# Kernel tuning notes

Hardware: AMD Instinct MI355X
Metric: run time of the kernel (lower is better)

## Reference

```python
import jax, jax.numpy as jnp
import numpy as np

N_NODES = 100000
N_EDGES = 1600000
HIDDEN = 128


def setup_inputs() -> dict:
    key = jax.random.key(0)
    ks = jax.random.split(key, 10)
    inp = {
        "hidden_states": jax.random.normal(ks[0], (N_NODES, HIDDEN), dtype=jnp.float32),
        "edges_i": jax.random.randint(ks[1], (2, N_EDGES), 0, N_NODES, dtype=jnp.int64),
        "edges_ii": jax.random.randint(ks[2], (2, N_EDGES), 0, N_NODES, dtype=jnp.int64),
        "edges_iii": jax.random.randint(ks[3], (2, N_EDGES), 0, N_NODES, dtype=jnp.int64),
        "edges_a": jax.random.randint(ks[4], (2, N_EDGES), 0, N_NODES, dtype=jnp.int64),
        # GCNConv weights (hidden -> hidden), no bias, Glorot-like init
        "W_i": jax.random.normal(ks[5], (HIDDEN, HIDDEN), dtype=jnp.float32) / np.sqrt(HIDDEN),
        "W_ii": jax.random.normal(ks[6], (HIDDEN, HIDDEN), dtype=jnp.float32) / np.sqrt(HIDDEN),
        "W_iii": jax.random.normal(ks[7], (HIDDEN, HIDDEN), dtype=jnp.float32) / np.sqrt(HIDDEN),
        "W_a": jax.random.normal(ks[8], (HIDDEN, HIDDEN), dtype=jnp.float32) / np.sqrt(HIDDEN),
    }
    return inp


def _gcn_conv(x, W, edges):
    # GCNConv with normalize=False, add_self_loops=False, bias=False:
    # out[dst] = sum over edges (x @ W)[src]
    xw = x @ W                                   # [N, H] small GEMM
    msg = jnp.take(xw, edges[0], axis=0)         # gather at src: [E, H]
    return jax.ops.segment_sum(msg, edges[1], num_segments=x.shape[0])


def reference(hidden_states, edges_i, edges_ii, edges_iii, edges_a, W_i, W_ii, W_iii, W_a):
    # VariationalNormalEpanechnikovDropout acts as identity in eval mode.
    x = hidden_states
    out = _gcn_conv(x, W_i, edges_i)
    out = out + _gcn_conv(x, W_ii, edges_ii)
    out = out + _gcn_conv(x, W_iii, edges_iii)
    out = out + _gcn_conv(x, W_a, edges_a)
    return out
```

## Files before the change

### kernel.cpp

```cpp
#include <hip/hip_runtime.h>


#define H 128
#define BSH 9
#define BNODES (1 << BSH)
#define SEGB (BNODES * 4)
#define EPB 16384

typedef __bf16 bf16x8 __attribute__((ext_vector_type(8)));
typedef float f32x4 __attribute__((ext_vector_type(4)));

static __device__ __forceinline__ ushort f2bf(float f) {
  union { float f; uint u; } v; v.f = f;
  uint r = (v.u + 0x7FFFu + ((v.u >> 16) & 1u)) >> 16;
  return (ushort)r;
}
static __device__ __forceinline__ float bflo(uint u) {
  union { uint u; float f; } v; v.u = u << 16; return v.f;
}
static __device__ __forceinline__ float bfhi(uint u) {
  union { uint u; float f; } v; v.u = u & 0xFFFF0000u; return v.f;
}

__global__ __launch_bounds__(256) void conv_prep(const float4* __restrict__ X4,
                                                 uint2* __restrict__ Xb2, int m,
                                                 const float* __restrict__ W0,
                                                 const float* __restrict__ W1,
                                                 const float* __restrict__ W2,
                                                 const float* __restrict__ W3,
                                                 ushort* __restrict__ Wt) {
  int i = blockIdx.x * 256 + threadIdx.x;
  if (i < m) {
    float4 v = X4[i];
    uint2 p;
    p.x = (uint)f2bf(v.x) | ((uint)f2bf(v.y) << 16);
    p.y = (uint)f2bf(v.z) | ((uint)f2bf(v.w) << 16);
    Xb2[i] = p;
  }
  if (i < 65536) {
    int kk = i & 127;
    int c = (i >> 7) & 127;
    int k = i >> 14;
    const float* W = (k == 0) ? W0 : (k == 1) ? W1 : (k == 2) ? W2 : W3;
    Wt[i] = f2bf(W[kk * 128 + c]);
  }
}

static __device__ __forceinline__ void fetch_edge(
    int gid, int c1, int c2, int c3,
    const int* d0, const int* d1, const int* d2, const int* d3,
    const int* s0, const int* s1, const int* s2, const int* s3,
    int& dst, int& src, int& k) {
  int i;
  const int *dp, *sp;
  if (gid < c1)      { k = 0; i = gid;      dp = d0; sp = s0; }
  else if (gid < c2) { k = 1; i = gid - c1; dp = d1; sp = s1; }
  else if (gid < c3) { k = 2; i = gid - c2; dp = d2; sp = s2; }
  else               { k = 3; i = gid - c3; dp = d3; sp = s3; }
  dst = dp[i];
  src = sp[i];
}

__global__ __launch_bounds__(256) void part_count(
    const int* __restrict__ d0, const int* __restrict__ d1,
    const int* __restrict__ d2, const int* __restrict__ d3,
    int c1, int c2, int c3, int tot, int nbin, int* __restrict__ hb) {
  __shared__ int lh[512];
  for (int i = threadIdx.x; i < nbin; i += 256) lh[i] = 0;
  __syncthreads();
  int base = blockIdx.x * EPB;
#pragma unroll 8
  for (int u = 0; u < EPB / 256; ++u) {
    int gid = base + u * 256 + threadIdx.x;
    if (gid < tot) {
      int i;
      const int* dp;
      if (gid < c1)      { i = gid;      dp = d0; }
      else if (gid < c2) { i = gid - c1; dp = d1; }
      else if (gid < c3) { i = gid - c2; dp = d2; }
      else               { i = gid - c3; dp = d3; }
      atomicAdd(&lh[dp[i] >> BSH], 1);
    }
  }
  __syncthreads();
  int* row = hb + (size_t)blockIdx.x * nbin;
  for (int i = threadIdx.x; i < nbin; i += 256) row[i] = lh[i];
}

__global__ __launch_bounds__(256) void part_scanA(int* __restrict__ hb,
                                                  int nblk, int nbin,
                                                  int* __restrict__ btot) {
  __shared__ int ws4[4];
  const int bin = blockIdx.x;
  const int t = threadIdx.x, lane = t & 63, wid = t >> 6;
  const int C = (nblk + 255) / 256;
  int b0 = t * C;
  int b1 = min(b0 + C, nblk);
  int s = 0;
  for (int b = b0; b < b1; ++b) s += hb[(size_t)b * nbin + bin];
  int incl = s;
#pragma unroll
  for (int d = 1; d < 64; d <<= 1) {
    int x = __shfl_up(incl, d, 64);
    if (lane >= d) incl += x;
  }
  if (lane == 63) ws4[wid] = incl;
  __syncthreads();
  if (t == 0) {
    int run = 0;
#pragma unroll
    for (int i = 0; i < 4; ++i) { int v = ws4[i]; ws4[i] = run; run += v; }
  }
  __syncthreads();
  int run = ws4[wid] + (incl - s);
  for (int b = b0; b < b1; ++b) {
    int v = hb[(size_t)b * nbin + bin];
    hb[(size_t)b * nbin + bin] = run;
    run += v;
  }
  if (t == 255) btot[bin] = run;
}

__global__ __launch_bounds__(512) void part_scanB(const int* __restrict__ btot,
                                                  int* __restrict__ binbase,
                                                  int nbin) {
  __shared__ int ws8[8];
  const int t = threadIdx.x, lane = t & 63, wid = t >> 6;
  int v = (t < nbin) ? btot[t] : 0;
  int incl = v;
#pragma unroll
  for (int d = 1; d < 64; d <<= 1) {
    int x = __shfl_up(incl, d, 64);
    if (lane >= d) incl += x;
  }
  if (lane == 63) ws8[wid] = incl;
  __syncthreads();
  if (t == 0) {
    int run = 0;
#pragma unroll
    for (int i = 0; i < 8; ++i) { int v2 = ws8[i]; ws8[i] = run; run += v2; }
  }
  __syncthreads();
  int excl = ws8[wid] + (incl - v);
  if (t < nbin) binbase[t] = excl;
  if (t == nbin - 1) binbase[nbin] = excl + v;
}

__global__ __launch_bounds__(256) void part_scatter(
    const int* __restrict__ d0, const int* __restrict__ d1,
    const int* __restrict__ d2, const int* __restrict__ d3,
    const int* __restrict__ s0, const int* __restrict__ s1,
    const int* __restrict__ s2, const int* __restrict__ s3,
    int c1, int c2, int c3, int tot, int nbin,
    const int* __restrict__ hb, const int* __restrict__ binbase,
    uint* __restrict__ part) {
  __shared__ int cur[512];
  const int* row = hb + (size_t)blockIdx.x * nbin;
  for (int i = threadIdx.x; i < nbin; i += 256) cur[i] = binbase[i] + row[i];
  __syncthreads();
  int base = blockIdx.x * EPB;
#pragma unroll 8
  for (int u = 0; u < EPB / 256; ++u) {
    int gid = base + u * 256 + threadIdx.x;
    if (gid < tot) {
      int dst, src, k;
      fetch_edge(gid, c1, c2, c3, d0, d1, d2, d3, s0, s1, s2, s3, dst, src, k);
      int pos = atomicAdd(&cur[dst >> BSH], 1);
      part[pos] = (uint)src | ((uint)(((dst & (BNODES - 1)) << 2) | k) << 17);
    }
  }
}

__global__ __launch_bounds__(1024) void build_bucket(
    const uint* __restrict__ part, const int* __restrict__ binbase,
    int* __restrict__ rp4, int* __restrict__ col_idx) {
  __shared__ int lh[SEGB];
  __shared__ int ws16[16];
  const int b = blockIdx.x;
  const int beg = binbase[b], end = binbase[b + 1];
  const int t = threadIdx.x, lane = t & 63, wid = t >> 6;

  lh[t] = 0;
  lh[t + 1024] = 0;
  __syncthreads();
  for (int i = beg + t; i < end; i += 1024)
    atomicAdd(&lh[part[i] >> 17], 1);
  __syncthreads();

  int v0 = lh[2 * t], v1 = lh[2 * t + 1];
  int s = v0 + v1;
  int incl = s;
#pragma unroll
  for (int d = 1; d < 64; d <<= 1) {
    int x = __shfl_up(incl, d, 64);
    if (lane >= d) incl += x;
  }
  if (lane == 63) ws16[wid] = incl;
  __syncthreads();
  if (t == 0) {
    int run = 0;
#pragma unroll
    for (int i = 0; i < 16; ++i) { int w = ws16[i]; ws16[i] = run; run += w; }
  }
  __syncthreads();
  int excl = beg + ws16[wid] + (incl - s);
  lh[2 * t] = excl;
  lh[2 * t + 1] = excl + v0;

  int gseg = b * SEGB + 2 * t;
  rp4[gseg] = excl;
  rp4[gseg + 1] = excl + v0;
  __syncthreads();

  for (int i = beg + t; i < end; i += 1024) {
    uint e = part[i];
    int pos = atomicAdd(&lh[e >> 17], 1);
    col_idx[pos] = (int)(e & 0x1FFFFu);
  }
}

#define ACC8(u)                                                       \
  do {                                                                \
    a0 += bflo((u).x); a1 += bfhi((u).x);                             \
    a2 += bflo((u).y); a3 += bfhi((u).y);                             \
    a4 += bflo((u).z); a5 += bfhi((u).z);                             \
    a6 += bflo((u).w); a7 += bfhi((u).w);                             \
  } while (0)

__global__ __launch_bounds__(256, 8) void gg(const uint* __restrict__ Xb,
                                             const int* __restrict__ rp4,
                                             const int* __restrict__ col_idx,
                                             const ushort* __restrict__ Wt,
                                             float* __restrict__ out, int n) {
  __shared__ uint sS[16][258];

  const int node0 = blockIdx.x * 16;
  const int wave = threadIdx.x >> 6;
  const int lane = threadIdx.x & 63;
  const int g = lane >> 4;
  const int qb = (lane & 15) * 4;

#pragma unroll 1
  for (int i = 0; i < 4; ++i) {
    int local = wave * 4 + i;
    int node = node0 + local;
    if (node < n) {
      const int4 rpv = *(const int4*)(rp4 + (size_t)node * 4);
      const int rpE = rp4[(size_t)node * 4 + 4];
      int pe0 = (rpv.x + lane < rpv.y) ? col_idx[rpv.x + lane] : 0;
      int pe1 = (rpv.y + lane < rpv.z) ? col_idx[rpv.y + lane] : 0;
      int pe2 = (rpv.z + lane < rpv.w) ? col_idx[rpv.z + lane] : 0;
      int pe3 = (rpv.w + lane < rpE)   ? col_idx[rpv.w + lane] : 0;
#pragma unroll
      for (int k = 0; k < 4; ++k) {
        int beg = (k == 0) ? rpv.x : (k == 1) ? rpv.y : (k == 2) ? rpv.z : rpv.w;
        int end = (k == 0) ? rpv.y : (k == 1) ? rpv.z : (k == 2) ? rpv.w : rpE;
        int pe  = (k == 0) ? pe0   : (k == 1) ? pe1   : (k == 2) ? pe2   : pe3;
        int len = end - beg;
        int m = (len > 64) ? 64 : len;
        float a0 = 0.f, a1 = 0.f, a2 = 0.f, a3 = 0.f;
        float a4 = 0.f, a5 = 0.f, a6 = 0.f, a7 = 0.f;
        int s = 0;
        for (; s + 16 <= m; s += 16) {
          int ea = __shfl(pe, s + g, 64);
          int eb = __shfl(pe, s + 4 + g, 64);
          int ec = __shfl(pe, s + 8 + g, 64);
          int ed = __shfl(pe, s + 12 + g, 64);
          uint4 ua = *(const uint4*)&Xb[(size_t)ea * 64 + qb];
          uint4 ub = *(const uint4*)&Xb[(size_t)eb * 64 + qb];
          uint4 uc = *(const uint4*)&Xb[(size_t)ec * 64 + qb];
          uint4 ud = *(const uint4*)&Xb[(size_t)ed * 64 + qb];
          ACC8(ua); ACC8(ub); ACC8(uc); ACC8(ud);
        }
        for (; s + 8 <= m; s += 8) {
          int ea = __shfl(pe, s + g, 64);
          int eb = __shfl(pe, s + 4 + g, 64);
          uint4 ua = *(const uint4*)&Xb[(size_t)ea * 64 + qb];
          uint4 ub = *(const uint4*)&Xb[(size_t)eb * 64 + qb];
          ACC8(ua); ACC8(ub);
        }
        for (; s < m; s += 4) {
          int li = s + g;
          int e = __shfl(pe, li, 64);
          if (li < m) {
            uint4 u = *(const uint4*)&Xb[(size_t)e * 64 + qb];
            ACC8(u);
          }
        }
        if (len > 64) {
          for (int j = beg + 64; j < end; j += 4) {
            int li = j + g;
            if (li < end) {
              int e = col_idx[li];
              uint4 u = *(const uint4*)&Xb[(size_t)e * 64 + qb];
              ACC8(u);
            }
          }
        }
        a0 += __shfl_xor(a0, 16, 64); a0 += __shfl_xor(a0, 32, 64);
        a1 += __shfl_xor(a1, 16, 64); a1 += __shfl_xor(a1, 32, 64);
        a2 += __shfl_xor(a2, 16, 64); a2 += __shfl_xor(a2, 32, 64);
        a3 += __shfl_xor(a3, 16, 64); a3 += __shfl_xor(a3, 32, 64);
        a4 += __shfl_xor(a4, 16, 64); a4 += __shfl_xor(a4, 32, 64);
        a5 += __shfl_xor(a5, 16, 64); a5 += __shfl_xor(a5, 32, 64);
        a6 += __shfl_xor(a6, 16, 64); a6 += __shfl_xor(a6, 32, 64);
        a7 += __shfl_xor(a7, 16, 64); a7 += __shfl_xor(a7, 32, 64);
        if (lane < 16) {
          uint* drow = &sS[local][k * 64 + qb];
          drow[0] = (uint)f2bf(a0) | ((uint)f2bf(a1) << 16);
          drow[1] = (uint)f2bf(a2) | ((uint)f2bf(a3) << 16);
          drow[2] = (uint)f2bf(a4) | ((uint)f2bf(a5) << 16);
          drow[3] = (uint)f2bf(a6) | ((uint)f2bf(a7) << 16);
        }
      }
    } else {
#pragma unroll
      for (int k = 0; k < 4; ++k) sS[local][k * 64 + lane] = 0u;
    }
  }
  __syncthreads();

  const ushort* sSu = (const ushort*)&sS[0][0];
  const int lr = lane & 15;
  const int lg = lane >> 4;
  const int cf0 = wave * 2;

  f32x4 acc0 = (f32x4)0.f, acc1 = (f32x4)0.f;

#pragma unroll
  for (int kc = 0; kc < 4; ++kc) {
#pragma unroll
    for (int k4 = 0; k4 < 4; ++k4) {
      bf16x8 a = *(const bf16x8*)&sSu[lr * 516 + kc * 128 + k4 * 32 + lg * 8];
      bf16x8 b0 = *(const bf16x8*)&Wt[kc * 16384 + (cf0 * 16 + lr) * 128 + k4 * 32 + lg * 8];
      bf16x8 b1 = *(const bf16x8*)&Wt[kc * 16384 + ((cf0 + 1) * 16 + lr) * 128 + k4 * 32 + lg * 8];
      acc0 = __builtin_amdgcn_mfma_f32_16x16x32_bf16(a, b0, acc0, 0, 0, 0);
      acc1 = __builtin_amdgcn_mfma_f32_16x16x32_bf16(a, b1, acc1, 0, 0, 0);
    }
  }

#pragma unroll
  for (int r = 0; r < 4; ++r) {
    int row = node0 + lg * 4 + r;
    if (row < n) {
      out[(size_t)row * H + cf0 * 16 + lr] = acc0[r];
      out[(size_t)row * H + (cf0 + 1) * 16 + lr] = acc1[r];
    }
  }
}

extern "C" void kernel_launch(void* const* d_in, const int* in_sizes, int n_in,
                              void* d_out, int out_size, void* d_ws, size_t ws_size,
                              hipStream_t stream) {
  const float* X = (const float*)d_in[0];
  const int* edges[4] = {(const int*)d_in[1], (const int*)d_in[2],
                         (const int*)d_in[3], (const int*)d_in[4]};
  const float* Wk[4] = {(const float*)d_in[5], (const float*)d_in[6],
                        (const float*)d_in[7], (const float*)d_in[8]};
  float* out = (float*)d_out;

  int n = in_sizes[0] / H;
  int nE[4];
  int tot = 0;
  for (int k = 0; k < 4; ++k) {
    nE[k] = in_sizes[1 + k] / 2;
    tot += nE[k];
  }
  int c1 = nE[0], c2 = c1 + nE[1], c3 = c2 + nE[2];
  int nbin = (n + BNODES - 1) >> BSH;
  int nblk = (tot + EPB - 1) / EPB;

  char* ws = (char*)d_ws;
  size_t off = 0;
  auto take = [&](size_t bytes) -> char* {
    char* p = ws + off;
    off = (off + bytes + 255) & ~(size_t)255;
    return p;
  };
  ushort* Wt = (ushort*)take(4 * 128 * 128 * sizeof(ushort));
  uint* Xb = (uint*)take((size_t)n * H * sizeof(ushort));
  int* hb = (int*)take((size_t)nblk * nbin * sizeof(int));
  int* btot = (int*)take((size_t)nbin * sizeof(int));
  int* binbase = (int*)take((size_t)(nbin + 1) * sizeof(int));
  int* rp4 = (int*)take(((size_t)nbin * SEGB + 1) * sizeof(int));
  uint* part = (uint*)take((size_t)tot * sizeof(uint));
  int* col_idx = (int*)take((size_t)tot * sizeof(int));

  const int* s0 = edges[0];
  const int* d0 = edges[0] + nE[0];
  const int* s1 = edges[1];
  const int* d1 = edges[1] + nE[1];
  const int* s2 = edges[2];
  const int* d2 = edges[2] + nE[2];
  const int* s3 = edges[3];
  const int* d3 = edges[3] + nE[3];

  conv_prep<<<(n * 32 + 255) / 256, 256, 0, stream>>>(
      (const float4*)X, (uint2*)Xb, n * 32, Wk[0], Wk[1], Wk[2], Wk[3], Wt);

  part_count<<<nblk, 256, 0, stream>>>(d0, d1, d2, d3, c1, c2, c3, tot, nbin, hb);
  part_scanA<<<nbin, 256, 0, stream>>>(hb, nblk, nbin, btot);
  part_scanB<<<1, 512, 0, stream>>>(btot, binbase, nbin);
  part_scatter<<<nblk, 256, 0, stream>>>(d0, d1, d2, d3, s0, s1, s2, s3,
                                         c1, c2, c3, tot, nbin, hb, binbase, part);
  build_bucket<<<nbin, 1024, 0, stream>>>(part, binbase, rp4, col_idx);

  gg<<<(n + 15) / 16, 256, 0, stream>>>(Xb, rp4, col_idx, Wt, out, n);
}
```

Baseline: 419.0 us.

## Slice feature dimension for cache-resident gathers and split gather from GEMM

Stores the bf16 node features as eight 16-feature slices, so each slice of the table is small enough to stay in cache. A new gather kernel assigns one slice per block, accumulates neighbor sums per relation and writes them to a workspace buffer. A separate MFMA GEMM kernel then multiplies the concatenated per-relation sums by a reordered stacked weight matrix, processing nodes in chunks sized to the free workspace. The trade-off is an extra global write and read of the intermediate sums, and each edge list is re-read once per slice, in exchange for better cache reuse on the random gathers.

```diff
diff --git a/kernel.cpp b/kernel.cpp
--- a/kernel.cpp
+++ b/kernel.cpp
@@ -22,27 +22,27 @@
   union { uint u; float f; } v; v.u = u & 0xFFFF0000u; return v.f;
 }
 
-__global__ __launch_bounds__(256) void conv_prep(const float4* __restrict__ X4,
-                                                 uint2* __restrict__ Xb2, int m,
-                                                 const float* __restrict__ W0,
-                                                 const float* __restrict__ W1,
-                                                 const float* __restrict__ W2,
-                                                 const float* __restrict__ W3,
-                                                 ushort* __restrict__ Wt) {
+__global__ __launch_bounds__(256) void conv_prep(
+    const float4* __restrict__ X4, uint2* __restrict__ Xb2v, int n,
+    const float* __restrict__ W0, const float* __restrict__ W1,
+    const float* __restrict__ W2, const float* __restrict__ W3,
+    ushort* __restrict__ Wt2) {
   int i = blockIdx.x * 256 + threadIdx.x;
+  int m = n * 32;
   if (i < m) {
+    int nd = i >> 5, fq = i & 31;
+    int s = fq >> 2;
     float4 v = X4[i];
     uint2 p;
     p.x = (uint)f2bf(v.x) | ((uint)f2bf(v.y) << 16);
     p.y = (uint)f2bf(v.z) | ((uint)f2bf(v.w) << 16);
-    Xb2[i] = p;
+    Xb2v[(size_t)(s * n + nd) * 4 + (fq & 3)] = p;
   }
   if (i < 65536) {
-    int kk = i & 127;
-    int c = (i >> 7) & 127;
-    int k = i >> 14;
+    int k = i >> 14, kk = (i >> 7) & 127, col = i & 127;
     const float* W = (k == 0) ? W0 : (k == 1) ? W1 : (k == 2) ? W2 : W3;
-    Wt[i] = f2bf(W[kk * 128 + c]);
+    int kidx = (kk >> 4) * 64 + k * 16 + (kk & 15);
+    Wt2[(size_t)col * 512 + kidx] = f2bf(W[kk * 128 + col]);
   }
 }
 
@@ -219,124 +219,115 @@
   }
 }
 
-#define ACC8(u)                                                       \
-  do {                                                                \
-    a0 += bflo((u).x); a1 += bfhi((u).x);                             \
-    a2 += bflo((u).y); a3 += bfhi((u).y);                             \
-    a4 += bflo((u).z); a5 += bfhi((u).z);                             \
-    a6 += bflo((u).w); a7 += bfhi((u).w);                             \
-  } while (0)
-
-__global__ __launch_bounds__(256, 8) void gg(const uint* __restrict__ Xb,
-                                             const int* __restrict__ rp4,
-                                             const int* __restrict__ col_idx,
-                                             const ushort* __restrict__ Wt,
-                                             float* __restrict__ out, int n) {
-  __shared__ uint sS[16][258];
-
-  const int node0 = blockIdx.x * 16;
+__global__ __launch_bounds__(256, 8) void gg_s(const uint* __restrict__ Xb2,
+                                               const int* __restrict__ rp4,
+                                               const int* __restrict__ col_idx,
+                                               uint* __restrict__ S2,
+                                               int n, int n0, int C) {
+  const int sl = blockIdx.x & 7;
+  const int node0 = n0 + (blockIdx.x >> 3) * 16;
+  const uint* Xs = Xb2 + (size_t)sl * n * 8;
+  uint* Ss = S2 + (size_t)sl * C * 32;
   const int wave = threadIdx.x >> 6;
   const int lane = threadIdx.x & 63;
-  const int g = lane >> 4;
-  const int qb = (lane & 15) * 4;
+  const int g = lane >> 3;
+  const int q = lane & 7;
 
 #pragma unroll 1
   for (int i = 0; i < 4; ++i) {
-    int local = wave * 4 + i;
-    int node = node0 + local;
-    if (node < n) {
-      const int4 rpv = *(const int4*)(rp4 + (size_t)node * 4);
-      const int rpE = rp4[(size_t)node * 4 + 4];
-      int pe0 = (rpv.x + lane < rpv.y) ? col_idx[rpv.x + lane] : 0;
-      int pe1 = (rpv.y + lane < rpv.z) ? col_idx[rpv.y + lane] : 0;
-      int pe2 = (rpv.z + lane < rpv.w) ? col_idx[rpv.z + lane] : 0;
-      int pe3 = (rpv.w + lane < rpE)   ? col_idx[rpv.w + lane] : 0;
-#pragma unroll
-      for (int k = 0; k < 4; ++k) {
-        int beg = (k == 0) ? rpv.x : (k == 1) ? rpv.y : (k == 2) ? rpv.z : rpv.w;
-        int end = (k == 0) ? rpv.y : (k == 1) ? rpv.z : (k == 2) ? rpv.w : rpE;
-        int pe  = (k == 0) ? pe0   : (k == 1) ? pe1   : (k == 2) ? pe2   : pe3;
-        int len = end - beg;
-        int m = (len > 64) ? 64 : len;
-        float a0 = 0.f, a1 = 0.f, a2 = 0.f, a3 = 0.f;
-        float a4 = 0.f, a5 = 0.f, a6 = 0.f, a7 = 0.f;
-        int s = 0;
-        for (; s + 16 <= m; s += 16) {
-          int ea = __shfl(pe, s + g, 64);
-          int eb = __shfl(pe, s + 4 + g, 64);
-          int ec = __shfl(pe, s + 8 + g, 64);
-          int ed = __shfl(pe, s + 12 + g, 64);
-          uint4 ua = *(const uint4*)&Xb[(size_t)ea * 64 + qb];
-          uint4 ub = *(const uint4*)&Xb[(size_t)eb * 64 + qb];
-          uint4 uc = *(const uint4*)&Xb[(size_t)ec * 64 + qb];
-          uint4 ud = *(const uint4*)&Xb[(size_t)ed * 64 + qb];
-          ACC8(ua); ACC8(ub); ACC8(uc); ACC8(ud);
+    int node = node0 + wave * 4 + i;
+    if (node >= n) continue;
+    const int4 rpv = *(const int4*)(rp4 + (size_t)node * 4);
+    const int rpE = rp4[(size_t)node * 4 + 4];
+    int pe0 = (rpv.x + lane < rpv.y) ? col_idx[rpv.x + lane] : 0;
+    int pe1 = (rpv.y + lane < rpv.z) ? col_idx[rpv.y + lane] : 0;
+    int pe2 = (rpv.z + lane < rpv.w) ? col_idx[rpv.z + lane] : 0;
+    int pe3 = (rpv.w + lane < rpE)   ? col_idx[rpv.w + lane] : 0;
+#pragma unroll
+    for (int k = 0; k < 4; ++k) {
+      int beg = (k == 0) ? rpv.x : (k == 1) ? rpv.y : (k == 2) ? rpv.z : rpv.w;
+      int end = (k == 0) ? rpv.y : (k == 1) ? rpv.z : (k == 2) ? rpv.w : rpE;
+      int p = (k == 0) ? pe0 : (k == 1) ? pe1 : (k == 2) ? pe2 : pe3;
+      int len = end - beg;
+      int m = (len > 64) ? 64 : len;
+      float a0 = 0.f, a1 = 0.f, b0 = 0.f, b1 = 0.f;
+      int t = 0;
+      for (; t + 16 <= m; t += 16) {
+        int ea = __shfl(p, t + g, 64);
+        int eb = __shfl(p, t + 8 + g, 64);
+        uint ua = Xs[(size_t)ea * 8 + q];
+        uint ub = Xs[(size_t)eb * 8 + q];
+        a0 += bflo(ua); a1 += bfhi(ua);
+        b0 += bflo(ub); b1 += bfhi(ub);
+      }
+      for (; t + 8 <= m; t += 8) {
+        int ea = __shfl(p, t + g, 64);
+        uint ua = Xs[(size_t)ea * 8 + q];
+        a0 += bflo(ua); a1 += bfhi(ua);
+      }
+      if (t < m) {
+        int li = t + g;
+        int e = __shfl(p, li, 64);
+        if (li < m) {
+          uint u = Xs[(size_t)e * 8 + q];
+          a0 += bflo(u); a1 += bfhi(u);
         }
-        for (; s + 8 <= m; s += 8) {
-          int ea = __shfl(pe, s + g, 64);
-          int eb = __shfl(pe, s + 4 + g, 64);
-          uint4 ua = *(const uint4*)&Xb[(size_t)ea * 64 + qb];
-          uint4 ub = *(const uint4*)&Xb[(size_t)eb * 64 + qb];
-          ACC8(ua); ACC8(ub);
-        }
-        for (; s < m; s += 4) {
-          int li = s + g;
-          int e = __shfl(pe, li, 64);
-          if (li < m) {
-            uint4 u = *(const uint4*)&Xb[(size_t)e * 64 + qb];
-            ACC8(u);
+      }
+      if (len > 64) {
+        for (int j = beg + 64; j < end; j += 8) {
+          int li = j + g;
+          if (li < end) {
+            int e = col_idx[li];
+            uint u = Xs[(size_t)e * 8 + q];
+            a0 += bflo(u); a1 += bfhi(u);
           }
         }
-        if (len > 64) {
-          for (int j = beg + 64; j < end; j += 4) {
-            int li = j + g;
-            if (li < end) {
-              int e = col_idx[li];
-              uint4 u = *(const uint4*)&Xb[(size_t)e * 64 + qb];
-              ACC8(u);
-            }
-          }
-        }
-        a0 += __shfl_xor(a0, 16, 64); a0 += __shfl_xor(a0, 32, 64);
-        a1 += __shfl_xor(a1, 16, 64); a1 += __shfl_xor(a1, 32, 64);
-        a2 += __shfl_xor(a2, 16, 64); a2 += __shfl_xor(a2, 32, 64);
-        a3 += __shfl_xor(a3, 16, 64); a3 += __shfl_xor(a3, 32, 64);
-        a4 += __shfl_xor(a4, 16, 64); a4 += __shfl_xor(a4, 32, 64);
-        a5 += __shfl_xor(a5, 16, 64); a5 += __shfl_xor(a5, 32, 64);
-        a6 += __shfl_xor(a6, 16, 64); a6 += __shfl_xor(a6, 32, 64);
-        a7 += __shfl_xor(a7, 16, 64); a7 += __shfl_xor(a7, 32, 64);
-        if (lane < 16) {
-          uint* drow = &sS[local][k * 64 + qb];
-          drow[0] = (uint)f2bf(a0) | ((uint)f2bf(a1) << 16);
-          drow[1] = (uint)f2bf(a2) | ((uint)f2bf(a3) << 16);
-          drow[2] = (uint)f2bf(a4) | ((uint)f2bf(a5) << 16);
-          drow[3] = (uint)f2bf(a6) | ((uint)f2bf(a7) << 16);
-        }
       }
-    } else {
-#pragma unroll
-      for (int k = 0; k < 4; ++k) sS[local][k * 64 + lane] = 0u;
+      float r0 = a0 + b0, r1 = a1 + b1;
+      r0 += __shfl_xor(r0, 8, 64);  r1 += __shfl_xor(r1, 8, 64);
+      r0 += __shfl_xor(r0, 16, 64); r1 += __shfl_xor(r1, 16, 64);
+      r0 += __shfl_xor(r0, 32, 64); r1 += __shfl_xor(r1, 32, 64);
+      if (g == 0)
+        Ss[(size_t)(node - n0) * 32 + k * 8 + q] =
+            (uint)f2bf(r0) | ((uint)f2bf(r1) << 16);
     }
   }
-  __syncthreads();
-
-  const ushort* sSu = (const ushort*)&sS[0][0];
+}
+
+__global__ __launch_bounds__(256) void gemm2(const uint* __restrict__ S2,
+                                             const ushort* __restrict__ Wt2,
+                                             float* __restrict__ out,
+                                             int n, int n0, int C) {
+  __shared__ __align__(16) ushort sA[16][516];
+
+  const int node0 = n0 + blockIdx.x * 16;
+  const int t = threadIdx.x;
+  uint* sAu = (uint*)&sA[0][0];
+
+#pragma unroll
+  for (int it = 0; it < 16; ++it) {
+    int s = it >> 1, h = it & 1;
+    int nd = h * 8 + (t >> 5);
+    int kq = t & 31;
+    uint v = S2[((size_t)s * C + (node0 - n0 + nd)) * 32 + kq];
+    sAu[nd * 258 + s * 32 + kq] = v;
+  }
+  __syncthreads();
+
+  const int lane = t & 63;
+  const int wave = t >> 6;
   const int lr = lane & 15;
   const int lg = lane >> 4;
   const int cf0 = wave * 2;
 
   f32x4 acc0 = (f32x4)0.f, acc1 = (f32x4)0.f;
-
-#pragma unroll
-  for (int kc = 0; kc < 4; ++kc) {
-#pragma unroll
-    for (int k4 = 0; k4 < 4; ++k4) {
-      bf16x8 a = *(const bf16x8*)&sSu[lr * 516 + kc * 128 + k4 * 32 + lg * 8];
-      bf16x8 b0 = *(const bf16x8*)&Wt[kc * 16384 + (cf0 * 16 + lr) * 128 + k4 * 32 + lg * 8];
-      bf16x8 b1 = *(const bf16x8*)&Wt[kc * 16384 + ((cf0 + 1) * 16 + lr) * 128 + k4 * 32 + lg * 8];
-      acc0 = __builtin_amdgcn_mfma_f32_16x16x32_bf16(a, b0, acc0, 0, 0, 0);
-      acc1 = __builtin_amdgcn_mfma_f32_16x16x32_bf16(a, b1, acc1, 0, 0, 0);
-    }
+#pragma unroll
+  for (int kc = 0; kc < 16; ++kc) {
+    bf16x8 a = *(const bf16x8*)&sA[lr][kc * 32 + lg * 8];
+    bf16x8 b0 = *(const bf16x8*)&Wt2[(size_t)(cf0 * 16 + lr) * 512 + kc * 32 + lg * 8];
+    bf16x8 b1 = *(const bf16x8*)&Wt2[(size_t)((cf0 + 1) * 16 + lr) * 512 + kc * 32 + lg * 8];
+    acc0 = __builtin_amdgcn_mfma_f32_16x16x32_bf16(a, b0, acc0, 0, 0, 0);
+    acc1 = __builtin_amdgcn_mfma_f32_16x16x32_bf16(a, b1, acc1, 0, 0, 0);
   }
 
 #pragma unroll
@@ -377,14 +368,22 @@
     off = (off + bytes + 255) & ~(size_t)255;
     return p;
   };
-  ushort* Wt = (ushort*)take(4 * 128 * 128 * sizeof(ushort));
-  uint* Xb = (uint*)take((size_t)n * H * sizeof(ushort));
+  ushort* Wt2 = (ushort*)take(128 * 512 * sizeof(ushort));
+  uint* Xb2 = (uint*)take((size_t)n * H * sizeof(ushort));
   int* hb = (int*)take((size_t)nblk * nbin * sizeof(int));
   int* btot = (int*)take((size_t)nbin * sizeof(int));
   int* binbase = (int*)take((size_t)(nbin + 1) * sizeof(int));
   int* rp4 = (int*)take(((size_t)nbin * SEGB + 1) * sizeof(int));
+  int* col_idx = (int*)take((size_t)tot * sizeof(int));
+  size_t part_off = off;
   uint* part = (uint*)take((size_t)tot * sizeof(uint));
-  int* col_idx = (int*)take((size_t)tot * sizeof(int));
+  uint* S2 = (uint*)(ws + part_off);
+  size_t s_avail = (ws_size > part_off) ? (ws_size - part_off) : 0;
+
+  long long cmax = (long long)(s_avail / 1024);
+  int chunk = (cmax > n) ? n : (int)cmax;
+  chunk &= ~15;
+  if (chunk < 16) chunk = 16;
 
   const int* s0 = edges[0];
   const int* d0 = edges[0] + nE[0];
@@ -396,7 +395,7 @@
   const int* d3 = edges[3] + nE[3];
 
   conv_prep<<<(n * 32 + 255) / 256, 256, 0, stream>>>(
-      (const float4*)X, (uint2*)Xb, n * 32, Wk[0], Wk[1], Wk[2], Wk[3], Wt);
+      (const float4*)X, (uint2*)Xb2, n, Wk[0], Wk[1], Wk[2], Wk[3], Wt2);
 
   part_count<<<nblk, 256, 0, stream>>>(d0, d1, d2, d3, c1, c2, c3, tot, nbin, hb);
   part_scanA<<<nbin, 256, 0, stream>>>(hb, nblk, nbin, btot);
@@ -405,5 +404,11 @@
                                          c1, c2, c3, tot, nbin, hb, binbase, part);
   build_bucket<<<nbin, 1024, 0, stream>>>(part, binbase, rp4, col_idx);
 
-  gg<<<(n + 15) / 16, 256, 0, stream>>>(Xb, rp4, col_idx, Wt, out, n);
-}
+  for (int n0 = 0; n0 < n; n0 += chunk) {
+    int c = n - n0;
+    if (c > chunk) c = chunk;
+    int tiles = (c + 15) / 16;
+    gg_s<<<tiles * 8, 256, 0, stream>>>(Xb2, rp4, col_idx, S2, n, n0, c);
+    gemm2<<<tiles, 256, 0, stream>>>(S2, Wt2, out, n, n0, c);
+  }
+}
```

Measured after the change: 715.1 us. 70.6% more time.
